# Kernel tuning notes

Hardware: AMD Instinct MI355X
Metric: run time of the kernel (lower is better)

## Reference

```python
import jax, jax.numpy as jnp
import numpy as np

B, H, W, DIM, NH = 2, 48, 48, 768, 12
HD = DIM // NH  # 64


def setup_inputs() -> dict:
    key = jax.random.key(0)
    ks = jax.random.split(key, 7)
    std = 0.02
    return {
        "x": jax.random.normal(ks[0], (B, H, W, DIM), jnp.float32),
        "rel_pos_h": jax.random.normal(ks[1], (2 * H - 1, HD), jnp.float32) * std,
        "rel_pos_w": jax.random.normal(ks[2], (2 * W - 1, HD), jnp.float32) * std,
        "qkv_w": jax.random.normal(ks[3], (3 * DIM, DIM), jnp.float32) * std,
        "qkv_b": jnp.zeros((3 * DIM,), jnp.float32),
        "proj_w": jax.random.normal(ks[4], (DIM, DIM), jnp.float32) * std,
        "proj_b": jnp.zeros((DIM,), jnp.float32),
    }


def reference(x, rel_pos_h, rel_pos_w, qkv_w, qkv_b, proj_w, proj_b):
    b, h, w, dim = x.shape
    nh = NH
    hd = dim // nh
    scale = hd ** -0.5
    n = h * w
    # qkv projection: (B,N,3*dim) -> (3, B*nh, N, hd)
    qkv = x.reshape(b, n, dim) @ qkv_w.T + qkv_b
    qkv = qkv.reshape(b, n, 3, nh, hd).transpose(2, 0, 3, 1, 4).reshape(3, b * nh, n, hd)
    q, k, v = qkv[0], qkv[1], qkv[2]
    # scaled dot-product scores (B*nh, N, N)
    attn = jnp.einsum('bnc,bmc->bnm', q * scale, k)
    # decomposed relative position bias (q_size == k_size, no interpolation)
    idx_h = jnp.arange(h)[:, None] - jnp.arange(h)[None, :] + (h - 1)  # (h,h)
    idx_w = jnp.arange(w)[:, None] - jnp.arange(w)[None, :] + (w - 1)  # (w,w)
    Rh = rel_pos_h[idx_h]  # (h, h, hd)
    Rw = rel_pos_w[idx_w]  # (w, w, hd)
    r_q = q.reshape(b * nh, h, w, hd)
    rel_h = jnp.einsum('bhwc,hkc->bhwk', r_q, Rh)  # (B*nh, h, w, h)
    rel_w = jnp.einsum('bhwc,wkc->bhwk', r_q, Rw)  # (B*nh, h, w, w)
    attn = (attn.reshape(b * nh, h, w, h, w)
            + rel_h[:, :, :, :, None]
            + rel_w[:, :, :, None, :]).reshape(b * nh, n, n)
    attn = jax.nn.softmax(attn, axis=-1)
    out = (attn @ v).reshape(b, nh, h, w, hd).transpose(0, 2, 3, 1, 4).reshape(b, h, w, dim)
    return out @ proj_w.T + proj_b
```

## Files before the change

### kernel.cpp

```cpp
#include <hip/hip_runtime.h>
#include <hip/hip_bf16.h>
#include <stdint.h>

#define NQ    2304
#define MROWS 4608
#define DIMC  768
#define NHEAD 12
#define HEADS 24
#define HD    64

typedef unsigned int uint;
typedef unsigned short u16;
typedef __attribute__((ext_vector_type(8))) short s16x8;
typedef __attribute__((ext_vector_type(4))) float f32x4;

#define MFMA16(a, b, c) __builtin_amdgcn_mfma_f32_16x16x32_bf16((a), (b), (c), 0, 0, 0)

static __device__ __forceinline__ float bfbits2f(uint u) {
  union { uint i; float f; } c; c.i = u << 16; return c.f;
}
static __device__ __forceinline__ u16 f2bf(float f) {
  __hip_bfloat16 h = __float2bfloat16(f);
  union { __hip_bfloat16 h; u16 u; } c; c.h = h; return c.u;
}
static __device__ __forceinline__ u16 f2h(float f) {
  union { _Float16 h; u16 u; } c; c.h = (_Float16)f; return c.u;
}
static __device__ __forceinline__ float h2f(u16 u) {
  union { u16 u; _Float16 h; } c; c.u = u; return (float)c.h;
}
static __device__ __forceinline__ void dec8(uint4 p, float* f) {
  f[0] = bfbits2f(p.x & 0xFFFFu); f[1] = bfbits2f(p.x >> 16);
  f[2] = bfbits2f(p.y & 0xFFFFu); f[3] = bfbits2f(p.y >> 16);
  f[4] = bfbits2f(p.z & 0xFFFFu); f[5] = bfbits2f(p.z >> 16);
  f[6] = bfbits2f(p.w & 0xFFFFu); f[7] = bfbits2f(p.w >> 16);
}
static __device__ __forceinline__ void ld8(const void* p, size_t idx, int bf, float* f) {
  if (bf) { dec8(*(const uint4*)((const u16*)p + idx), f); }
  else {
    const float4* q = (const float4*)((const float*)p + idx);
    float4 a = q[0], b = q[1];
    f[0] = a.x; f[1] = a.y; f[2] = a.z; f[3] = a.w;
    f[4] = b.x; f[5] = b.y; f[6] = b.z; f[7] = b.w;
  }
}
static __device__ __forceinline__ float ld1(const void* p, size_t idx, int bf) {
  return bf ? bfbits2f(((const u16*)p)[idx]) : ((const float*)p)[idx];
}
static __device__ __forceinline__ uint4 ld8_to_bf(const void* p, size_t idx, int bf) {
  if (bf) return *(const uint4*)((const u16*)p + idx);
  float f[8]; ld8(p, idx, 0, f);
  uint4 u;
  u.x = (uint)f2bf(f[0]) | ((uint)f2bf(f[1]) << 16);
  u.y = (uint)f2bf(f[2]) | ((uint)f2bf(f[3]) << 16);
  u.z = (uint)f2bf(f[4]) | ((uint)f2bf(f[5]) << 16);
  u.w = (uint)f2bf(f[6]) | ((uint)f2bf(f[7]) << 16);
  return u;
}

__global__ __launch_bounds__(64) void detect_k(const u16* __restrict__ x,
                                               int* __restrict__ mode) {
  int t = threadIdx.x;
  int cnt = 0;
  for (int i = 0; i < 32; ++i) {
    uint u = x[(size_t)(t * 32 + i) * 2];
    uint e = (u >> 7) & 0xFFu;
    uint mag = u & 0x7FFFu;
    if (mag == 0 || (e >= 113 && e <= 133)) cnt++;
  }
#pragma unroll
  for (int d = 1; d < 64; d <<= 1) cnt += __shfl_xor(cnt, d);
  if (t == 0) mode[0] = (cnt > 1024) ? 1 : 0;
}

__global__ __launch_bounds__(256) void qkv_gemm_k(
    const void* __restrict__ Xp, const void* __restrict__ Wp,
    const void* __restrict__ Bq, const int* __restrict__ mode,
    u16* __restrict__ Q, u16* __restrict__ K, u16* __restrict__ Vt)
{
  __shared__ __align__(16) u16 As[128][40];
  __shared__ __align__(16) u16 Bs[128][40];
  const int bf = mode[0];
  const int t = threadIdx.x;
  const int w = t >> 6, l15 = t & 15, quad = (t >> 4) & 3;
  const int wr = w >> 1, wc = w & 1;
  const int row0 = blockIdx.y << 7, col0 = blockIdx.x << 7;
  const int lr = t >> 1, lk = (t & 1) << 4;

  f32x4 zero4 = {0.f, 0.f, 0.f, 0.f};
  f32x4 acc[4][4];
#pragma unroll
  for (int i = 0; i < 4; ++i)
#pragma unroll
    for (int j = 0; j < 4; ++j) acc[i][j] = zero4;

  for (int kt = 0; kt < DIMC; kt += 32) {
    __syncthreads();
    *(uint4*)&As[lr][lk]     = ld8_to_bf(Xp, (size_t)(row0 + lr) * DIMC + kt + lk, bf);
    *(uint4*)&As[lr][lk + 8] = ld8_to_bf(Xp, (size_t)(row0 + lr) * DIMC + kt + lk + 8, bf);
    *(uint4*)&Bs[lr][lk]     = ld8_to_bf(Wp, (size_t)(col0 + lr) * DIMC + kt + lk, bf);
    *(uint4*)&Bs[lr][lk + 8] = ld8_to_bf(Wp, (size_t)(col0 + lr) * DIMC + kt + lk + 8, bf);
    __syncthreads();
    s16x8 af[4], bfr[4];
#pragma unroll
    for (int i = 0; i < 4; ++i)
      af[i] = *(const s16x8*)&As[(wr << 6) + (i << 4) + l15][quad << 3];
#pragma unroll
    for (int j = 0; j < 4; ++j)
      bfr[j] = *(const s16x8*)&Bs[(wc << 6) + (j << 4) + l15][quad << 3];
#pragma unroll
    for (int i = 0; i < 4; ++i)
#pragma unroll
      for (int j = 0; j < 4; ++j)
        acc[i][j] = MFMA16(af[i], bfr[j], acc[i][j]);
  }

#pragma unroll
  for (int jt = 0; jt < 4; ++jt) {
    int col = col0 + (wc << 6) + (jt << 4) + l15;
    int which = col / DIMC;
    int rem = col - which * DIMC;
    int head = rem >> 6, d = rem & 63;
    float bv = ld1(Bq, col, bf);
#pragma unroll
    for (int i = 0; i < 4; ++i)
#pragma unroll
      for (int r = 0; r < 4; ++r) {
        int mrow = row0 + (wr << 6) + (i << 4) + (quad << 2) + r;
        int b_ = (mrow >= NQ) ? 1 : 0;
        int n = mrow - b_ * NQ;
        u16 val = f2bf(acc[i][jt][r] + bv);
        size_t bh = (size_t)(b_ * NHEAD + head);
        if (which == 2)      Vt[(bh * HD + d) * NQ + n] = val;
        else if (which == 1) K[(bh * NQ + n) * HD + d] = val;
        else                 Q[(bh * NQ + n) * HD + d] = val;
      }
  }
}

__global__ __launch_bounds__(256) void bias_gemm_k(
    const u16* __restrict__ Qw,
    const void* __restrict__ rph, const void* __restrict__ rpw,
    const int* __restrict__ mode,
    u16* __restrict__ Bh_g, u16* __restrict__ Bw_g)
{
  __shared__ __align__(16) u16 As[128][72];
  __shared__ __align__(16) u16 Bs[192][72];
  const int bf = mode[0];
  const int t = threadIdx.x;
  const int w = t >> 6, l15 = t & 15, quad = (t >> 4) & 3;
  const int wr = w >> 1, wc = w & 1;
  const int blk = blockIdx.x;
  const int bhd = blk / 18;
  const int row0 = (blk - bhd * 18) << 7;

  {
    int lr = t >> 1, lk = (t & 1) << 5;
    const u16* src = Qw + ((size_t)bhd * NQ + row0 + lr) * HD + lk;
    *(uint4*)&As[lr][lk]      = *(const uint4*)(src);
    *(uint4*)&As[lr][lk + 8]  = *(const uint4*)(src + 8);
    *(uint4*)&As[lr][lk + 16] = *(const uint4*)(src + 16);
    *(uint4*)&As[lr][lk + 24] = *(const uint4*)(src + 24);
  }
  for (int e = t; e < 384; e += 256) {
    int row = e >> 1, k32 = (e & 1) << 5;
    int tab = (row >= 96) ? 1 : 0;
    int r2 = row - (tab ? 96 : 0);
    if (r2 > 94) r2 = 0;
    const void* src = tab ? rpw : rph;
    *(uint4*)&Bs[row][k32]      = ld8_to_bf(src, (size_t)r2 * HD + k32, bf);
    *(uint4*)&Bs[row][k32 + 8]  = ld8_to_bf(src, (size_t)r2 * HD + k32 + 8, bf);
    *(uint4*)&Bs[row][k32 + 16] = ld8_to_bf(src, (size_t)r2 * HD + k32 + 16, bf);
    *(uint4*)&Bs[row][k32 + 24] = ld8_to_bf(src, (size_t)r2 * HD + k32 + 24, bf);
  }
  __syncthreads();

  f32x4 zero4 = {0.f, 0.f, 0.f, 0.f};
  f32x4 acc[4][6];
#pragma unroll
  for (int i = 0; i < 4; ++i)
#pragma unroll
    for (int j = 0; j < 6; ++j) acc[i][j] = zero4;

#pragma unroll
  for (int ks = 0; ks < 2; ++ks) {
    s16x8 af[4], bfr[6];
#pragma unroll
    for (int i = 0; i < 4; ++i)
      af[i] = *(const s16x8*)&As[(wr << 6) + (i << 4) + l15][(ks << 5) + (quad << 3)];
#pragma unroll
    for (int j = 0; j < 6; ++j)
      bfr[j] = *(const s16x8*)&Bs[wc * 96 + (j << 4) + l15][(ks << 5) + (quad << 3)];
#pragma unroll
    for (int i = 0; i < 4; ++i)
#pragma unroll
      for (int j = 0; j < 6; ++j)
        acc[i][j] = MFMA16(af[i], bfr[j], acc[i][j]);
  }

#pragma unroll
  for (int jt = 0; jt < 6; ++jt) {
    int col = wc * 96 + (jt << 4) + l15;
    int tab = (col >= 96) ? 1 : 0;
    int j = col - (tab ? 96 : 0);
    if (j >= 95) continue;
    u16* dstT = tab ? Bw_g : Bh_g;
#pragma unroll
    for (int i = 0; i < 4; ++i)
#pragma unroll
      for (int r = 0; r < 4; ++r) {
        int n = row0 + (wr << 6) + (i << 4) + (quad << 2) + r;
        int qh = (n * 10923) >> 19;
        int coord = tab ? (n - qh * 48) : qh;
        int c = coord + 47 - j;
        if (c >= 0 && c < 48)
          dstT[((size_t)bhd * 48 + c) * NQ + n] = f2h(acc[i][jt][r]);
      }
  }
}

__global__ __launch_bounds__(256) void attn_k(
    const u16* __restrict__ Qw, const u16* __restrict__ Kw,
    const u16* __restrict__ Vtg,
    const u16* __restrict__ Bh_g, const u16* __restrict__ Bw_g,
    int S, float* __restrict__ Opart, float* __restrict__ Lpart,
    u16* __restrict__ Aout)
{
  __shared__ __align__(16) u16 BhL[48][256];
  __shared__ __align__(16) u16 BwL[256][52];

  const int bid = blockIdx.x;
  const int xcd = bid & 7;
  const int local = bid >> 3;
  const int per_head = 9 * S;
  const int head_l = local / per_head;
  const int rem = local - head_l * per_head;
  const int qb = rem / S;
  const int z = rem - qb * S;
  const int bhd = xcd * 3 + head_l;
  const int q0 = qb << 8;
  const int span = NQ / S;
  const int kt_lo = z * span, kt_hi = kt_lo + span;

  const int t = threadIdx.x;
  const int w = t >> 6, l15 = t & 15, quad = (t >> 4) & 3;
  const float scale = 0.125f;

  const u16* kbase  = Kw  + (size_t)bhd * NQ * HD;
  const u16* vtbase = Vtg + (size_t)bhd * HD * NQ;
  const int q0w = q0 + (w << 6);

  for (int e = t; e < 1536; e += 256) {
    int c = e >> 5;
    int off = (e & 31) << 3;
    size_t gi = ((size_t)bhd * 48 + c) * NQ + q0 + off;
    *(uint4*)&BhL[c][off] = *(const uint4*)(Bh_g + gi);
    uint4 wv = *(const uint4*)(Bw_g + gi);
    u16 vals[8];
    vals[0] = wv.x & 0xFFFFu; vals[1] = wv.x >> 16;
    vals[2] = wv.y & 0xFFFFu; vals[3] = wv.y >> 16;
    vals[4] = wv.z & 0xFFFFu; vals[5] = wv.z >> 16;
    vals[6] = wv.w & 0xFFFFu; vals[7] = wv.w >> 16;
#pragma unroll
    for (int j = 0; j < 8; ++j) BwL[off + j][c] = vals[j];
  }

  s16x8 qa0[4], qa1[4];
#pragma unroll
  for (int g = 0; g < 4; ++g) {
    const u16* qfrag = Qw + ((size_t)bhd * NQ + q0w + (g << 4) + l15) * HD + (quad << 3);
    qa0[g] = *(const s16x8*)(qfrag);
    qa1[g] = *(const s16x8*)(qfrag + 32);
  }

  __syncthreads();

  f32x4 zero4 = {0.f, 0.f, 0.f, 0.f};
  f32x4 acc_o[4][4];
#pragma unroll
  for (int g = 0; g < 4; ++g)
#pragma unroll
    for (int nc = 0; nc < 4; ++nc) acc_o[g][nc] = zero4;
  float l_st[4] = {0.f, 0.f, 0.f, 0.f};
  const int srcA = ((quad & 1) << 5) + l15;
  const int srcB = srcA + 16;
  const int hi = quad >> 1;
  int km = 0;

  for (int kt0 = kt_lo; kt0 < kt_hi; kt0 += 64) {
    int kh0 = (kt0 * 10923) >> 19;
    int thr = (kh0 + 1) * 48 - kt0;

#pragma unroll
    for (int h = 0; h < 2; ++h) {
      uint W[4][4];
#pragma unroll
      for (int nc2 = 0; nc2 < 2; ++nc2) {
        int nc = (h << 1) + nc2;
        const u16* kp = kbase + (size_t)(kt0 + (nc << 4) + l15) * HD + (quad << 3);
        s16x8 kb0 = *(const s16x8*)(kp);
        s16x8 kb1 = *(const s16x8*)(kp + 32);
        int bnc = km + (nc << 4);
        bnc = (bnc >= 48) ? bnc - 48 : bnc;
        int kl = (nc << 4) + (quad << 2);
#pragma unroll
        for (int g = 0; g < 4; ++g) {
          f32x4 a = MFMA16(kb0, qa0[g], zero4);
          f32x4 s4 = MFMA16(kb1, qa1[g], a);
          int qrl = (w << 6) + (g << 4) + l15;
          float bh0v = h2f(BhL[kh0][qrl]);
          float bh1v = h2f(BhL[kh0 + 1][qrl]);
          uint2 pv = *(const uint2*)&BwL[qrl][bnc + (quad << 2)];
          float b0 = h2f((u16)(pv.x & 0xFFFFu));
          float b1 = h2f((u16)(pv.x >> 16));
          float b2 = h2f((u16)(pv.y & 0xFFFFu));
          float b3 = h2f((u16)(pv.y >> 16));
          float e0 = __expf(s4[0] * scale + ((kl     >= thr) ? bh1v : bh0v) + b0);
          float e1 = __expf(s4[1] * scale + ((kl + 1 >= thr) ? bh1v : bh0v) + b1);
          float e2 = __expf(s4[2] * scale + ((kl + 2 >= thr) ? bh1v : bh0v) + b2);
          float e3 = __expf(s4[3] * scale + ((kl + 3 >= thr) ? bh1v : bh0v) + b3);
          l_st[g] += (e0 + e1) + (e2 + e3);
          W[g][2 * nc2]     = (uint)f2bf(e0) | ((uint)f2bf(e1) << 16);
          W[g][2 * nc2 + 1] = (uint)f2bf(e2) | ((uint)f2bf(e3) << 16);
        }
      }
      s16x8 vb[4];
#pragma unroll
      for (int nc = 0; nc < 4; ++nc)
        vb[nc] = *(const s16x8*)(vtbase + (size_t)((nc << 4) + l15) * NQ
                                 + kt0 + (h << 5) + (quad << 3));
#pragma unroll
      for (int g = 0; g < 4; ++g) {
        uint e0 = __shfl(W[g][0], srcA), e1 = __shfl(W[g][1], srcA);
        uint e2 = __shfl(W[g][2], srcA), e3 = __shfl(W[g][3], srcA);
        uint g0 = __shfl(W[g][0], srcB), g1 = __shfl(W[g][1], srcB);
        uint g2 = __shfl(W[g][2], srcB), g3 = __shfl(W[g][3], srcB);
        union { uint u[4]; s16x8 v; } pf;
        pf.u[0] = hi ? e2 : e0; pf.u[1] = hi ? e3 : e1;
        pf.u[2] = hi ? g2 : g0; pf.u[3] = hi ? g3 : g1;
#pragma unroll
        for (int nc = 0; nc < 4; ++nc)
          acc_o[g][nc] = MFMA16(pf.v, vb[nc], acc_o[g][nc]);
      }
    }
    km += 16;
    if (km >= 48) km -= 48;
  }

#pragma unroll
  for (int g = 0; g < 4; ++g) {
    float lg = l_st[g];
    lg += __shfl_xor(lg, 16);
    lg += __shfl_xor(lg, 32);
    if (S > 1) {
      float* Op = Opart + ((size_t)(z * HEADS + bhd) * NQ + q0) * HD;
#pragma unroll
      for (int r = 0; r < 4; ++r) {
        int row = (w << 6) + (g << 4) + (quad << 2) + r;
#pragma unroll
        for (int nc = 0; nc < 4; ++nc)
          Op[(size_t)row * HD + (nc << 4) + l15] = acc_o[g][nc][r];
      }
      if (quad == 0)
        Lpart[(size_t)(z * HEADS + bhd) * NQ + q0w + (g << 4) + l15] = lg;
    } else {
      int b_ = bhd / NHEAD, head = bhd - b_ * NHEAD;
      float invl = 1.f / lg;
      int bsrc = (quad << 4) + (quad << 2);
#pragma unroll
      for (int r = 0; r < 4; ++r) {
        float inv = __shfl(invl, bsrc + r);
        int token = q0 + (w << 6) + (g << 4) + (quad << 2) + r;
        u16* dst = Aout + ((size_t)b_ * NQ + token) * DIMC + (head << 6);
#pragma unroll
        for (int nc = 0; nc < 4; ++nc)
          dst[(nc << 4) + l15] = f2bf(acc_o[g][nc][r] * inv);
      }
    }
  }
}

__global__ __launch_bounds__(256) void combine_k(
    const float* __restrict__ Op, const float* __restrict__ Lp,
    int S, u16* __restrict__ Aout)
{
  int idx = blockIdx.x * 256 + threadIdx.x;
  int m = idx / 192;
  int cq = idx - m * 192;
  int ccol = cq << 2;
  int head = ccol >> 6, d0 = ccol & 63;
  int b_ = (m >= NQ) ? 1 : 0;
  int n = m - b_ * NQ;
  int bh = b_ * NHEAD + head;
  float ox = 0.f, oy = 0.f, oz = 0.f, ow = 0.f, ls = 0.f;
  for (int zz = 0; zz < S; ++zz) {
    const float* ob = Op + ((size_t)(zz * HEADS + bh) * NQ + n) * HD + d0;
    float4 v = *(const float4*)ob;
    ox += v.x; oy += v.y; oz += v.z; ow += v.w;
    ls += Lp[(size_t)(zz * HEADS + bh) * NQ + n];
  }
  float inv = 1.f / ls;
  u16* dst = Aout + (size_t)m * DIMC + ccol;
  dst[0] = f2bf(ox * inv); dst[1] = f2bf(oy * inv);
  dst[2] = f2bf(oz * inv); dst[3] = f2bf(ow * inv);
}

__global__ __launch_bounds__(256) void proj_gemm_k(
    const u16* __restrict__ A, const void* __restrict__ Wp,
    const void* __restrict__ Bp, const int* __restrict__ mode,
    void* __restrict__ Out)
{
  __shared__ __align__(16) u16 As[128][40];
  __shared__ __align__(16) u16 Bs[128][40];
  const int bf = mode[0];
  const int t = threadIdx.x;
  const int w = t >> 6, l15 = t & 15, quad = (t >> 4) & 3;
  const int wr = w >> 1, wc = w & 1;
  const int row0 = blockIdx.y << 7, col0 = blockIdx.x << 7;
  const int lr = t >> 1, lk = (t & 1) << 4;

  f32x4 zero4 = {0.f, 0.f, 0.f, 0.f};
  f32x4 acc[4][4];
#pragma unroll
  for (int i = 0; i < 4; ++i)
#pragma unroll
    for (int j = 0; j < 4; ++j) acc[i][j] = zero4;

  for (int kt = 0; kt < DIMC; kt += 32) {
    __syncthreads();
    *(uint4*)&As[lr][lk]     = *(const uint4*)(A + (size_t)(row0 + lr) * DIMC + kt + lk);
    *(uint4*)&As[lr][lk + 8] = *(const uint4*)(A + (size_t)(row0 + lr) * DIMC + kt + lk + 8);
    *(uint4*)&Bs[lr][lk]     = ld8_to_bf(Wp, (size_t)(col0 + lr) * DIMC + kt + lk, bf);
    *(uint4*)&Bs[lr][lk + 8] = ld8_to_bf(Wp, (size_t)(col0 + lr) * DIMC + kt + lk + 8, bf);
    __syncthreads();
    s16x8 af[4], bfr[4];
#pragma unroll
    for (int i = 0; i < 4; ++i)
      af[i] = *(const s16x8*)&As[(wr << 6) + (i << 4) + l15][quad << 3];
#pragma unroll
    for (int j = 0; j < 4; ++j)
      bfr[j] = *(const s16x8*)&Bs[(wc << 6) + (j << 4) + l15][quad << 3];
#pragma unroll
    for (int i = 0; i < 4; ++i)
#pragma unroll
      for (int j = 0; j < 4; ++j)
        acc[i][j] = MFMA16(af[i], bfr[j], acc[i][j]);
  }

#pragma unroll
  for (int jt = 0; jt < 4; ++jt) {
    int col = col0 + (wc << 6) + (jt << 4) + l15;
    float bv = ld1(Bp, col, bf);
#pragma unroll
    for (int i = 0; i < 4; ++i)
#pragma unroll
      for (int r = 0; r < 4; ++r) {
        int mrow = row0 + (wr << 6) + (i << 4) + (quad << 2) + r;
        float val = acc[i][jt][r] + bv;
        size_t off = (size_t)mrow * DIMC + col;
        if (bf) ((u16*)Out)[off] = f2bf(val);
        else    ((float*)Out)[off] = val;
      }
  }
}

extern "C" void kernel_launch(void* const* d_in, const int* in_sizes, int n_in,
                              void* d_out, int out_size, void* d_ws, size_t ws_size,
                              hipStream_t stream)
{
  const void* x    = d_in[0];
  const void* rph  = d_in[1];
  const void* rpw  = d_in[2];
  const void* qkvw = d_in[3];
  const void* qkvb = d_in[4];
  const void* pw   = d_in[5];
  const void* pb   = d_in[6];

  int* mode = (int*)d_ws;
  const size_t qkv_elems = (size_t)HEADS * NQ * HD;
  u16* q    = (u16*)((char*)d_ws + 16);
  u16* k    = q + qkv_elems;
  u16* vt   = k + qkv_elems;
  u16* aout = vt + qkv_elems;
  const size_t base = 16 + 4 * qkv_elems * 2;
  const size_t biasElems = (size_t)HEADS * 48 * NQ;
  u16* bh_g = (u16*)((char*)d_ws + base);
  u16* bw_g = bh_g + biasElems;
  const size_t base2 = base + 2 * biasElems * 2;
  const size_t perO = (size_t)HEADS * NQ * HD * 4;
  const size_t perL = (size_t)HEADS * NQ * 4;

  int S = 1;
  if (ws_size >= base2 + 3 * (perO + perL)) S = 3;
  else if (ws_size >= base2 + 2 * (perO + perL)) S = 2;
  float* opart = (float*)((char*)d_ws + base2);
  float* lpart = (float*)((char*)d_ws + base2 + (size_t)S * perO);

  detect_k<<<1, 64, 0, stream>>>((const u16*)x, mode);
  qkv_gemm_k<<<dim3(18, 36), 256, 0, stream>>>(x, qkvw, qkvb, mode, q, k, vt);
  bias_gemm_k<<<dim3(432), 256, 0, stream>>>(q, rph, rpw, mode, bh_g, bw_g);
  attn_k<<<dim3(216 * S), 256, 0, stream>>>(q, k, vt, bh_g, bw_g,
                                            S, opart, lpart, aout);
  if (S > 1)
    combine_k<<<dim3(3456), 256, 0, stream>>>(opart, lpart, S, aout);
  proj_gemm_k<<<dim3(6, 36), 256, 0, stream>>>(aout, pw, pb, mode, d_out);
}
```

Baseline: 385.5 us.

## Pre-convert inputs to bf16 and transpose V in a separate kernel

Adds a conversion kernel that turns x, qkv weights and proj weights into bf16 once, so the GEMMs load bf16 directly instead of converting fp32 in every tile load. The QKV GEMM epilogue now writes V row-major with coalesced stores, and a new LDS-tiled kernel transposes it into Vt in place of the scattered strided stores. The workspace is re-laid out so the bf16 buffers reuse the partial-output region. This adds two launches and extra global traffic in exchange for cheaper GEMM loads and coalesced writes. The detect kernel is widened to 256 threads.

```diff
diff --git a/kernel.cpp b/kernel.cpp
--- a/kernel.cpp
+++ b/kernel.cpp
@@ -58,25 +58,49 @@
   return u;
 }
 
-__global__ __launch_bounds__(64) void detect_k(const u16* __restrict__ x,
-                                               int* __restrict__ mode) {
+__global__ __launch_bounds__(256) void detect_k(const u16* __restrict__ x,
+                                                int* __restrict__ mode) {
+  __shared__ int wsum[4];
   int t = threadIdx.x;
   int cnt = 0;
-  for (int i = 0; i < 32; ++i) {
-    uint u = x[(size_t)(t * 32 + i) * 2];
+  for (int i = 0; i < 8; ++i) {
+    uint u = x[(size_t)(t * 8 + i) * 2];
     uint e = (u >> 7) & 0xFFu;
     uint mag = u & 0x7FFFu;
     if (mag == 0 || (e >= 113 && e <= 133)) cnt++;
   }
 #pragma unroll
   for (int d = 1; d < 64; d <<= 1) cnt += __shfl_xor(cnt, d);
-  if (t == 0) mode[0] = (cnt > 1024) ? 1 : 0;
+  if ((t & 63) == 0) wsum[t >> 6] = cnt;
+  __syncthreads();
+  if (t == 0) mode[0] = ((wsum[0] + wsum[1] + wsum[2] + wsum[3]) > 1024) ? 1 : 0;
+}
+
+#define NX8 442368u
+#define NW8 221184u
+#define NP8 73728u
+__global__ __launch_bounds__(256) void convert_k(
+    const void* __restrict__ x, const void* __restrict__ qkvw,
+    const void* __restrict__ pw, const int* __restrict__ mode,
+    u16* __restrict__ xb, u16* __restrict__ wb, u16* __restrict__ pwb)
+{
+  const int bf = mode[0];
+  uint i8 = blockIdx.x * 256 + threadIdx.x;
+  if (i8 < NX8) {
+    *(uint4*)(xb + (size_t)i8 * 8) = ld8_to_bf(x, (size_t)i8 * 8, bf);
+  } else if (i8 < NX8 + NW8) {
+    size_t j = i8 - NX8;
+    *(uint4*)(wb + j * 8) = ld8_to_bf(qkvw, j * 8, bf);
+  } else if (i8 < NX8 + NW8 + NP8) {
+    size_t j = i8 - NX8 - NW8;
+    *(uint4*)(pwb + j * 8) = ld8_to_bf(pw, j * 8, bf);
+  }
 }
 
 __global__ __launch_bounds__(256) void qkv_gemm_k(
-    const void* __restrict__ Xp, const void* __restrict__ Wp,
+    const u16* __restrict__ Xb, const u16* __restrict__ Wb,
     const void* __restrict__ Bq, const int* __restrict__ mode,
-    u16* __restrict__ Q, u16* __restrict__ K, u16* __restrict__ Vt)
+    u16* __restrict__ Q, u16* __restrict__ K, u16* __restrict__ V)
 {
   __shared__ __align__(16) u16 As[128][40];
   __shared__ __align__(16) u16 Bs[128][40];
@@ -96,10 +120,10 @@
 
   for (int kt = 0; kt < DIMC; kt += 32) {
     __syncthreads();
-    *(uint4*)&As[lr][lk]     = ld8_to_bf(Xp, (size_t)(row0 + lr) * DIMC + kt + lk, bf);
-    *(uint4*)&As[lr][lk + 8] = ld8_to_bf(Xp, (size_t)(row0 + lr) * DIMC + kt + lk + 8, bf);
-    *(uint4*)&Bs[lr][lk]     = ld8_to_bf(Wp, (size_t)(col0 + lr) * DIMC + kt + lk, bf);
-    *(uint4*)&Bs[lr][lk + 8] = ld8_to_bf(Wp, (size_t)(col0 + lr) * DIMC + kt + lk + 8, bf);
+    *(uint4*)&As[lr][lk]     = *(const uint4*)(Xb + (size_t)(row0 + lr) * DIMC + kt + lk);
+    *(uint4*)&As[lr][lk + 8] = *(const uint4*)(Xb + (size_t)(row0 + lr) * DIMC + kt + lk + 8);
+    *(uint4*)&Bs[lr][lk]     = *(const uint4*)(Wb + (size_t)(col0 + lr) * DIMC + kt + lk);
+    *(uint4*)&Bs[lr][lk + 8] = *(const uint4*)(Wb + (size_t)(col0 + lr) * DIMC + kt + lk + 8);
     __syncthreads();
     s16x8 af[4], bfr[4];
 #pragma unroll
@@ -122,6 +146,7 @@
     int rem = col - which * DIMC;
     int head = rem >> 6, d = rem & 63;
     float bv = ld1(Bq, col, bf);
+    u16* dst = (which == 0) ? Q : (which == 1) ? K : V;
 #pragma unroll
     for (int i = 0; i < 4; ++i)
 #pragma unroll
@@ -129,12 +154,34 @@
         int mrow = row0 + (wr << 6) + (i << 4) + (quad << 2) + r;
         int b_ = (mrow >= NQ) ? 1 : 0;
         int n = mrow - b_ * NQ;
-        u16 val = f2bf(acc[i][jt][r] + bv);
-        size_t bh = (size_t)(b_ * NHEAD + head);
-        if (which == 2)      Vt[(bh * HD + d) * NQ + n] = val;
-        else if (which == 1) K[(bh * NQ + n) * HD + d] = val;
-        else                 Q[(bh * NQ + n) * HD + d] = val;
-      }
+        dst[(((size_t)(b_ * NHEAD + head)) * NQ + n) * HD + d] = f2bf(acc[i][jt][r] + bv);
+      }
+  }
+}
+
+__global__ __launch_bounds__(256) void vtrans_k(
+    const u16* __restrict__ V, u16* __restrict__ Vt)
+{
+  __shared__ __align__(16) u16 L[64][72];
+  const int blk = blockIdx.x;
+  const int bhd = blk / 36;
+  const int n0 = (blk - bhd * 36) << 6;
+  const int t = threadIdx.x;
+  const int r = t >> 3, c8 = (t & 7) << 3;
+
+  const u16* src = V + ((size_t)bhd * NQ + n0) * HD;
+  *(uint4*)&L[r][c8]      = *(const uint4*)(src + (size_t)r * HD + c8);
+  *(uint4*)&L[r + 32][c8] = *(const uint4*)(src + (size_t)(r + 32) * HD + c8);
+  __syncthreads();
+
+  u16* dst = Vt + (size_t)bhd * HD * NQ + n0;
+#pragma unroll
+  for (int half = 0; half < 2; ++half) {
+    int d = r + (half << 5);
+    u16 tmp[8];
+#pragma unroll
+    for (int j = 0; j < 8; ++j) tmp[j] = L[c8 + j][d];
+    *(uint4*)(dst + (size_t)d * NQ + c8) = *(uint4*)tmp;
   }
 }
 
@@ -406,7 +453,7 @@
 }
 
 __global__ __launch_bounds__(256) void proj_gemm_k(
-    const u16* __restrict__ A, const void* __restrict__ Wp,
+    const u16* __restrict__ A, const u16* __restrict__ Wb,
     const void* __restrict__ Bp, const int* __restrict__ mode,
     void* __restrict__ Out)
 {
@@ -430,8 +477,8 @@
     __syncthreads();
     *(uint4*)&As[lr][lk]     = *(const uint4*)(A + (size_t)(row0 + lr) * DIMC + kt + lk);
     *(uint4*)&As[lr][lk + 8] = *(const uint4*)(A + (size_t)(row0 + lr) * DIMC + kt + lk + 8);
-    *(uint4*)&Bs[lr][lk]     = ld8_to_bf(Wp, (size_t)(col0 + lr) * DIMC + kt + lk, bf);
-    *(uint4*)&Bs[lr][lk + 8] = ld8_to_bf(Wp, (size_t)(col0 + lr) * DIMC + kt + lk + 8, bf);
+    *(uint4*)&Bs[lr][lk]     = *(const uint4*)(Wb + (size_t)(col0 + lr) * DIMC + kt + lk);
+    *(uint4*)&Bs[lr][lk + 8] = *(const uint4*)(Wb + (size_t)(col0 + lr) * DIMC + kt + lk + 8);
     __syncthreads();
     s16x8 af[4], bfr[4];
 #pragma unroll
@@ -478,30 +525,41 @@
 
   int* mode = (int*)d_ws;
   const size_t qkv_elems = (size_t)HEADS * NQ * HD;
+  const size_t NXe = (size_t)MROWS * DIMC;
+  const size_t NWe = (size_t)3 * DIMC * DIMC;
+  const size_t NPe = (size_t)DIMC * DIMC;
   u16* q    = (u16*)((char*)d_ws + 16);
   u16* k    = q + qkv_elems;
   u16* vt   = k + qkv_elems;
   u16* aout = vt + qkv_elems;
-  const size_t base = 16 + 4 * qkv_elems * 2;
+  u16* v    = aout;
+  u16* pwb  = aout + qkv_elems;
   const size_t biasElems = (size_t)HEADS * 48 * NQ;
-  u16* bh_g = (u16*)((char*)d_ws + base);
+  u16* bh_g = pwb + NPe;
   u16* bw_g = bh_g + biasElems;
-  const size_t base2 = base + 2 * biasElems * 2;
+  char* R   = (char*)(bw_g + biasElems);
+  const size_t baseR = (size_t)((char*)R - (char*)d_ws);
+  u16* xb = (u16*)R;
+  u16* wb = xb + NXe;
+  const size_t needXW = (NXe + NWe) * 2;
   const size_t perO = (size_t)HEADS * NQ * HD * 4;
   const size_t perL = (size_t)HEADS * NQ * 4;
 
   int S = 1;
-  if (ws_size >= base2 + 3 * (perO + perL)) S = 3;
-  else if (ws_size >= base2 + 2 * (perO + perL)) S = 2;
-  float* opart = (float*)((char*)d_ws + base2);
-  float* lpart = (float*)((char*)d_ws + base2 + (size_t)S * perO);
-
-  detect_k<<<1, 64, 0, stream>>>((const u16*)x, mode);
-  qkv_gemm_k<<<dim3(18, 36), 256, 0, stream>>>(x, qkvw, qkvb, mode, q, k, vt);
+  size_t n3 = 3 * (perO + perL), n2 = 2 * (perO + perL), n1 = perO + perL;
+  if (ws_size >= baseR + (n3 > needXW ? n3 : needXW)) S = 3;
+  else if (ws_size >= baseR + (n2 > needXW ? n2 : needXW)) S = 2;
+  float* opart = (float*)R;
+  float* lpart = (float*)(R + (size_t)S * perO);
+
+  detect_k<<<1, 256, 0, stream>>>((const u16*)x, mode);
+  convert_k<<<dim3(2880), 256, 0, stream>>>(x, qkvw, pw, mode, xb, wb, pwb);
+  qkv_gemm_k<<<dim3(18, 36), 256, 0, stream>>>(xb, wb, qkvb, mode, q, k, v);
+  vtrans_k<<<dim3(864), 256, 0, stream>>>(v, vt);
   bias_gemm_k<<<dim3(432), 256, 0, stream>>>(q, rph, rpw, mode, bh_g, bw_g);
   attn_k<<<dim3(216 * S), 256, 0, stream>>>(q, k, vt, bh_g, bw_g,
                                             S, opart, lpart, aout);
   if (S > 1)
     combine_k<<<dim3(3456), 256, 0, stream>>>(opart, lpart, S, aout);
-  proj_gemm_k<<<dim3(6, 36), 256, 0, stream>>>(aout, pw, pb, mode, d_out);
-}
+  proj_gemm_k<<<dim3(6, 36), 256, 0, stream>>>(aout, pwb, pb, mode, d_out);
+}
```

Result: faster. 344.5 us (-10.6%).
